# Performance work log

Hardware: AMD Instinct MI355X
Metric: run time of the kernel (lower is better)

The kernel has to match this reference:

```python
import jax, jax.numpy as jnp
import numpy as np

B, S, H = 2, 2048, 2048
NH, HD = 16, 128


def rotate_half(x):
    x1, x2 = x[..., : x.shape[-1] // 2], x[..., x.shape[-1] // 2 :]
    return jnp.concatenate((-x2, x1), axis=-1)


def setup_inputs() -> dict:
    key = jax.random.key(0)
    ks = jax.random.split(key, 8)
    return {
        "hidden": jax.random.normal(ks[0], (B, S, H), dtype=jnp.float32),
        "cos": jax.random.uniform(ks[1], (S, HD), dtype=jnp.float32),
        "sin": jax.random.uniform(ks[2], (S, HD), dtype=jnp.float32),
        "attention_mask": jnp.zeros((B, 1, S, S), dtype=jnp.float32),
        "Wq": jax.random.normal(ks[3], (H, H), dtype=jnp.float32) * 0.02,
        "Wk": jax.random.normal(ks[4], (H, H), dtype=jnp.float32) * 0.02,
        "Wv": jax.random.normal(ks[5], (H, H), dtype=jnp.float32) * 0.02,
        "Wo": jax.random.normal(ks[6], (H, H), dtype=jnp.float32) * 0.02,
    }


def reference(hidden, cos, sin, attention_mask, Wq, Wk, Wv, Wo):
    b, s, h = hidden.shape
    # torch Linear: y = x @ W.T ; reshape to [B, NH, S, HD]
    def proj(W):
        return (hidden @ W.T).reshape(b, s, NH, HD).transpose(0, 2, 1, 3)

    q, k, v = proj(Wq), proj(Wk), proj(Wv)
    c = cos[None, None, :, :]  # [1,1,S,HD]
    si = sin[None, None, :, :]
    q = q * c + rotate_half(q) * si
    k = k * c + rotate_half(k) * si
    scores = jnp.einsum("bhqd,bhkd->bhqk", q, k) / jnp.sqrt(jnp.float32(HD))
    scores = scores + attention_mask
    attn = jax.nn.softmax(scores.astype(jnp.float32), axis=-1).astype(q.dtype)
    out = jnp.einsum("bhqk,bhkd->bhqd", attn, v)
    out = out.transpose(0, 2, 1, 3).reshape(b, s, h)
    return out @ Wo.T
```

## Files before the change

kernel.cpp:

```cpp
#include <hip/hip_runtime.h>
#include <hip/hip_bf16.h>
#include <math.h>

#define SEQ 2048
#define HID 2048
#define NHEAD 16
#define HDIM 128
#define LDQ 6144

typedef __bf16 bf16_t;
typedef __bf16 bf16x2 __attribute__((ext_vector_type(2)));
typedef __bf16 bf16x4_t __attribute__((ext_vector_type(4)));
typedef __bf16 bf16x8 __attribute__((ext_vector_type(8)));
typedef float f32x4 __attribute__((ext_vector_type(4)));
typedef float f32x16 __attribute__((ext_vector_type(16)));
typedef unsigned u32x4 __attribute__((ext_vector_type(4)));

#define MFMA16(a, b, c) __builtin_amdgcn_mfma_f32_16x16x32_bf16(a, b, c, 0, 0, 0)
#define MFMA32(a, b, c) __builtin_amdgcn_mfma_f32_32x32x16_bf16(a, b, c, 0, 0, 0)
#define GLOAD_LDS(g, l) \
  __builtin_amdgcn_global_load_lds((const __attribute__((address_space(1))) void*)(g), \
                                   (__attribute__((address_space(3))) void*)(l), 16, 0, 0)

static __device__ inline unsigned pk2(float lo, float hi) {
  bf16x2 t; t[0] = (bf16_t)lo; t[1] = (bf16_t)hi;
  return __builtin_bit_cast(unsigned, t);
}

__global__ void cast_hidden(const float* __restrict__ in, bf16_t* __restrict__ out) {
  int i = blockIdx.x * 256 + threadIdx.x;
  float4 v = ((const float4*)in)[i];
  bf16x4_t b;
  b[0] = (bf16_t)v.x; b[1] = (bf16_t)v.y; b[2] = (bf16_t)v.z; b[3] = (bf16_t)v.w;
  ((bf16x4_t*)out)[i] = b;
}

__global__ void cast_weights(const float* __restrict__ a, const float* __restrict__ b,
                             const float* __restrict__ c, const float* __restrict__ d,
                             bf16_t* __restrict__ out) {
  const float* srcs[4] = {a, b, c, d};
  const float* src = srcs[blockIdx.y];
  bf16_t* dst = out + (size_t)blockIdx.y * (HID * HID);
  int i = blockIdx.x * 256 + threadIdx.x;
  float4 v = ((const float4*)src)[i];
  bf16x4_t o;
  o[0] = (bf16_t)v.x; o[1] = (bf16_t)v.y; o[2] = (bf16_t)v.z; o[3] = (bf16_t)v.w;
  ((bf16x4_t*)dst)[i] = o;
}

__global__ __launch_bounds__(256, 3) void gemm_bt(
    const bf16_t* __restrict__ A, const bf16_t* __restrict__ Bw,
    bf16_t* __restrict__ Cb, float* __restrict__ Cf,
    int M, int N, int K) {
  __shared__ bf16_t As[2][128 * 32];
  __shared__ bf16_t Bs[2][128 * 32];
  const int tid = threadIdx.x;
  const int lane = tid & 63, wid = tid >> 6;
  const int wr = wid >> 1, wc = wid & 1;
  const int lr = lane & 15, lg = lane >> 4;
  const int nwg = gridDim.x;
  const int lid = (blockIdx.x & 7) * (nwg >> 3) + (blockIdx.x >> 3);
  const int nbc = N >> 7;
  const int brow = lid / nbc, bcol = lid % nbc;

  f32x4 acc[4][4] = {};

  const int srow = tid >> 2, sch = tid & 3;
#define GSTAGE(k0, bb)                                                                   \
  {                                                                                      \
    _Pragma("unroll") for (int is = 0; is < 2; ++is) {                                   \
      int row = srow + is * 64;                                                          \
      GLOAD_LDS(A + (size_t)(brow * 128 + row) * K + (k0) + sch * 8,                     \
                &As[bb][(row * 4 + sch) * 8]);                                           \
      GLOAD_LDS(Bw + (size_t)(bcol * 128 + row) * K + (k0) + sch * 8,                    \
                &Bs[bb][(row * 4 + sch) * 8]);                                           \
    }                                                                                    \
  }

  GSTAGE(0, 0);
  __syncthreads();

  const int nt = K / 32;
  for (int t = 0; t < nt; ++t) {
    const int cb = t & 1;
    if (t + 1 < nt) GSTAGE((t + 1) * 32, cb ^ 1);
    bf16x8 af[4], bfr[4];
#pragma unroll
    for (int m = 0; m < 4; ++m)
      af[m] = *(const bf16x8*)(&As[cb][(wr * 64 + m * 16 + lr) * 32 + lg * 8]);
#pragma unroll
    for (int n = 0; n < 4; ++n)
      bfr[n] = *(const bf16x8*)(&Bs[cb][(wc * 64 + n * 16 + lr) * 32 + lg * 8]);
#pragma unroll
    for (int m = 0; m < 4; ++m)
#pragma unroll
      for (int n = 0; n < 4; ++n)
        acc[m][n] = MFMA16(af[m], bfr[n], acc[m][n]);
    __syncthreads();
  }
#undef GSTAGE

#pragma unroll
  for (int m = 0; m < 4; ++m)
#pragma unroll
    for (int n = 0; n < 4; ++n)
#pragma unroll
      for (int r = 0; r < 4; ++r) {
        int row = brow * 128 + wr * 64 + m * 16 + lg * 4 + r;
        int col = bcol * 128 + wc * 64 + n * 16 + lr;
        float v = acc[m][n][r];
        if (Cf) Cf[(size_t)row * N + col] = v;
        else    Cb[(size_t)row * N + col] = (bf16_t)v;
      }
}

__global__ void rope_qk(bf16_t* __restrict__ QKV,
                        const float* __restrict__ cost, const float* __restrict__ sint) {
  const float SCALE = 0.08838834764831845f;
  int idx = blockIdx.x * 256 + threadIdx.x;
  int d8 = idx & 7;
  int t = idx >> 3;
  int h = t & 15;
  int row = t >> 4;
  int s = row & (SEQ - 1);
  size_t base = (size_t)row * LDQ + h * HDIM;
  const float4* cp = (const float4*)(cost + s * HDIM);
  const float4* sp = (const float4*)(sint + s * HDIM);
  float4 c0a = cp[d8 * 2], c0b = cp[d8 * 2 + 1];
  float4 c1a = cp[16 + d8 * 2], c1b = cp[16 + d8 * 2 + 1];
  float4 s0a = sp[d8 * 2], s0b = sp[d8 * 2 + 1];
  float4 s1a = sp[16 + d8 * 2], s1b = sp[16 + d8 * 2 + 1];
  float c0[8] = {c0a.x, c0a.y, c0a.z, c0a.w, c0b.x, c0b.y, c0b.z, c0b.w};
  float c1[8] = {c1a.x, c1a.y, c1a.z, c1a.w, c1b.x, c1b.y, c1b.z, c1b.w};
  float s0[8] = {s0a.x, s0a.y, s0a.z, s0a.w, s0b.x, s0b.y, s0b.z, s0b.w};
  float s1[8] = {s1a.x, s1a.y, s1a.z, s1a.w, s1b.x, s1b.y, s1b.z, s1b.w};

  bf16_t* Q = QKV;
  bf16_t* K = QKV + 2048;
  bf16x8 qlo = *(bf16x8*)(Q + base + d8 * 8);
  bf16x8 qhi = *(bf16x8*)(Q + base + 64 + d8 * 8);
  bf16x8 klo = *(bf16x8*)(K + base + d8 * 8);
  bf16x8 khi = *(bf16x8*)(K + base + 64 + d8 * 8);
  bf16x8 qlo2, qhi2, klo2, khi2;
#pragma unroll
  for (int j = 0; j < 8; ++j) {
    float q0 = (float)qlo[j], q1 = (float)qhi[j];
    qlo2[j] = (bf16_t)((q0 * c0[j] - q1 * s0[j]) * SCALE);
    qhi2[j] = (bf16_t)((q1 * c1[j] + q0 * s1[j]) * SCALE);
    float k0 = (float)klo[j], k1 = (float)khi[j];
    klo2[j] = (bf16_t)(k0 * c0[j] - k1 * s0[j]);
    khi2[j] = (bf16_t)(k1 * c1[j] + k0 * s1[j]);
  }
  *(bf16x8*)(Q + base + d8 * 8) = qlo2;
  *(bf16x8*)(Q + base + 64 + d8 * 8) = qhi2;
  *(bf16x8*)(K + base + d8 * 8) = klo2;
  *(bf16x8*)(K + base + 64 + d8 * 8) = khi2;
}

__global__ void transpose_v(const bf16_t* __restrict__ Vf, bf16_t* __restrict__ Vt) {
  __shared__ bf16_t t[32][33];
  int tx = threadIdx.x & 31, ty = threadIdx.x >> 5;
  int r0 = blockIdx.y * 32, c0 = blockIdx.x * 32;
#pragma unroll
  for (int j = 0; j < 4; ++j)
    t[ty + j * 8][tx] = Vf[(size_t)(r0 + ty + j * 8) * LDQ + c0 + tx];
  __syncthreads();
#pragma unroll
  for (int j = 0; j < 4; ++j) {
    int c = c0 + ty + j * 8;
    int r = r0 + tx;
    int h = c >> 7, d = c & 127, b = r >> 11, s = r & (SEQ - 1);
    Vt[(((size_t)(b * NHEAD + h)) * HDIM + d) * SEQ + s] = t[tx][ty + j * 8];
  }
}

__global__ __launch_bounds__(512, 2) void flash_fwd(
    const bf16_t* __restrict__ Qf, const bf16_t* __restrict__ Kf,
    const bf16_t* __restrict__ Vt, const float* __restrict__ mask,
    bf16_t* __restrict__ AO) {
  __shared__ char smem[131072];
  char* KsB = smem;
  char* VsB = smem + 65536;
  const int tid = threadIdx.x, lane = tid & 63, wid = tid >> 6;
  const int q32 = lane & 31, hi = lane >> 5;

  const int x = blockIdx.x;
  const int bh = x & 31, qt = x >> 5;
  const int b = bh >> 4, h = bh & 15;
  const int qg = qt * 256 + wid * 32 + q32;

  bf16x8 qf[8];
  const bf16_t* qptr = Qf + (size_t)(b * SEQ + qg) * LDQ + h * HDIM + hi * 8;
#pragma unroll
  for (int ds = 0; ds < 8; ++ds) qf[ds] = *(const bf16x8*)(qptr + ds * 16);

  const float* mp = mask + (size_t)b * SEQ * SEQ + (size_t)qg * SEQ + hi * 4;

  float mrun = -INFINITY, lpart = 0.f;
  f32x16 o[4] = {};

#define STAGE_KV(kt_, bb)                                                                \
  {                                                                                      \
    const int kb0_ = (kt_) * 128;                                                        \
    _Pragma("unroll") for (int is = 0; is < 4; ++is) {                                   \
      int p = tid + is * 512;                                                            \
      int row = p >> 4, ch = p & 15;                                                     \
      int src = (ch * 16) ^ ((row & 7) << 4);                                            \
      GLOAD_LDS((const char*)(Kf + (size_t)(b * SEQ + kb0_ + row) * LDQ + h * HDIM) +    \
                    src,                                                                 \
                KsB + (bb) * 32768 + p * 16);                                            \
      GLOAD_LDS((const char*)(Vt + (size_t)(bh * HDIM + row) * SEQ + kb0_) + src,        \
                VsB + (bb) * 32768 + p * 16);                                            \
    }                                                                                    \
  }

  STAGE_KV(0, 0);
  __syncthreads();

  const int NT = SEQ / 128;
  for (int kt = 0; kt < NT; ++kt) {
    const int cur = kt & 1;
    const int kb0 = kt * 128;
    if (kt + 1 < NT) STAGE_KV(kt + 1, cur ^ 1);

#pragma unroll
    for (int kb = 0; kb < 4; ++kb) {
      f32x16 sacc;
#pragma unroll
      for (int g = 0; g < 4; ++g) {
        float4 m4 = *(const float4*)(mp + kb0 + kb * 32 + 8 * g);
        sacc[4 * g + 0] = m4.x; sacc[4 * g + 1] = m4.y;
        sacc[4 * g + 2] = m4.z; sacc[4 * g + 3] = m4.w;
      }
#pragma unroll
      for (int ds = 0; ds < 8; ++ds) {
        int row = kb * 32 + q32;
        bf16x8 kfr = *(const bf16x8*)(KsB + cur * 32768 + row * 256 +
                                      ((ds * 32 + hi * 16) ^ ((row & 7) << 4)));
        sacc = MFMA32(kfr, qf[ds], sacc);
      }

      float mx = sacc[0];
#pragma unroll
      for (int r = 1; r < 16; ++r) mx = fmaxf(mx, sacc[r]);
      mx = fmaxf(mx, __shfl_xor(mx, 32, 64));
      if (!__all(mx <= mrun + 8.f)) {
        float mnew = fmaxf(mrun, mx);
        float corr = __expf(mrun - mnew);
        mrun = mnew;
        lpart *= corr;
#pragma unroll
        for (int d0 = 0; d0 < 4; ++d0)
#pragma unroll
          for (int r = 0; r < 16; ++r) o[d0][r] *= corr;
      }

      float p[16];
      float rs = 0.f;
#pragma unroll
      for (int r = 0; r < 16; ++r) {
        p[r] = __expf(sacc[r] - mrun);
        rs += p[r];
      }
      lpart += rs;

#pragma unroll
      for (int s = 0; s < 2; ++s) {
        unsigned A1 = pk2(p[8 * s + 0], p[8 * s + 1]);
        unsigned A2 = pk2(p[8 * s + 2], p[8 * s + 3]);
        unsigned B1 = pk2(p[8 * s + 4], p[8 * s + 5]);
        unsigned B2 = pk2(p[8 * s + 6], p[8 * s + 7]);
        unsigned A1s = __shfl_xor(A1, 32, 64);
        unsigned A2s = __shfl_xor(A2, 32, 64);
        unsigned B1s = __shfl_xor(B1, 32, 64);
        unsigned B2s = __shfl_xor(B2, 32, 64);
        unsigned w0 = hi ? B1s : A1;
        unsigned w1 = hi ? B2s : A2;
        unsigned w2 = hi ? B1 : A1s;
        unsigned w3 = hi ? B2 : A2s;
        u32x4 W = {w0, w1, w2, w3};
        bf16x8 pav = __builtin_bit_cast(bf16x8, W);
        const int gs = kb * 2 + s;
#pragma unroll
        for (int d0 = 0; d0 < 4; ++d0) {
          int vrow = d0 * 32 + q32;
          bf16x8 vf = *(const bf16x8*)(VsB + cur * 32768 + vrow * 256 +
                                       ((gs * 32 + hi * 16) ^ ((vrow & 7) << 4)));
          o[d0] = MFMA32(vf, pav, o[d0]);
        }
      }
    }
    __syncthreads();
  }
#undef STAGE_KV

  float l = lpart + __shfl_xor(lpart, 32, 64);
  float rl = 1.f / l;
  bf16_t* aorow = AO + (size_t)(b * SEQ + qg) * HID + h * HDIM;
#pragma unroll
  for (int d0 = 0; d0 < 4; ++d0)
#pragma unroll
    for (int g = 0; g < 4; ++g) {
      unsigned lo = pk2(o[d0][4 * g + 0] * rl, o[d0][4 * g + 1] * rl);
      unsigned hi2 = pk2(o[d0][4 * g + 2] * rl, o[d0][4 * g + 3] * rl);
      int d = d0 * 32 + 8 * g + 4 * hi;
      *(unsigned*)(aorow + d) = lo;
      *(unsigned*)(aorow + d + 2) = hi2;
    }
}

extern "C" void kernel_launch(void* const* d_in, const int* in_sizes, int n_in,
                              void* d_out, int out_size, void* d_ws, size_t ws_size,
                              hipStream_t stream) {
  const float* hidden = (const float*)d_in[0];
  const float* cost   = (const float*)d_in[1];
  const float* sint   = (const float*)d_in[2];
  const float* mask   = (const float*)d_in[3];
  const float* Wq     = (const float*)d_in[4];
  const float* Wk     = (const float*)d_in[5];
  const float* Wv     = (const float*)d_in[6];
  const float* Wo     = (const float*)d_in[7];
  float* out = (float*)d_out;
  char* ws = (char*)d_ws;

  bf16_t* Af  = (bf16_t*)(ws + 0);
  bf16_t* Wqb = (bf16_t*)(ws + 16777216);
  bf16_t* Wob = (bf16_t*)(ws + 41943040);
  bf16_t* QKV = (bf16_t*)(ws + 50331648);
  bf16_t* Vt  = (bf16_t*)(ws + 0);
  bf16_t* AO  = (bf16_t*)(ws + 16777216);

  cast_hidden<<<8192, 256, 0, stream>>>(hidden, Af);
  cast_weights<<<dim3(4096, 4), 256, 0, stream>>>(Wq, Wk, Wv, Wo, Wqb);

  gemm_bt<<<1536, 256, 0, stream>>>(Af, Wqb, QKV, nullptr, 4096, LDQ, HID);

  rope_qk<<<2048, 256, 0, stream>>>(QKV, cost, sint);
  transpose_v<<<dim3(64, 128), 256, 0, stream>>>(QKV + 4096, Vt);

  flash_fwd<<<256, 512, 0, stream>>>(QKV, QKV + 2048, Vt, mask, AO);

  gemm_bt<<<512, 256, 0, stream>>>(AO, Wob, nullptr, out, 4096, HID, HID);
}
```

Before: 331.4 us.

## Use 256x256-tile 8-wave pipelined GEMM for fused QKV projection

Adds a new GEMM kernel with 256x256 output tiles, 512 threads, 128KB LDS double buffering with XOR swizzle, and a phased schedule that interleaves half-tile global-to-LDS loads with MFMA work using setprio and explicit waitcnt/barriers. The QKV projection is switched to it, cutting the grid from 1536 to 384 blocks. Larger tiles raise arithmetic intensity and reduce global/LDS traffic per FLOP. The trade-off is lower occupancy, only 384 blocks on 256 CUs which may leave load imbalance, and fragile hand-tuned wait counts.

Result: faster. 324.8 us (-2.0%).

```diff
diff --git a/kernel.cpp b/kernel.cpp
--- a/kernel.cpp
+++ b/kernel.cpp
@@ -46,6 +46,101 @@
   bf16x4_t o;
   o[0] = (bf16_t)v.x; o[1] = (bf16_t)v.y; o[2] = (bf16_t)v.z; o[3] = (bf16_t)v.w;
   ((bf16x4_t*)dst)[i] = o;
+}
+
+__global__ __launch_bounds__(512, 2) void gemm256(
+    const bf16_t* __restrict__ A, const bf16_t* __restrict__ Bw,
+    bf16_t* __restrict__ Cb, float* __restrict__ Cf, int M, int N, int K) {
+  __shared__ char smem[131072];
+  const int tid = threadIdx.x, lane = tid & 63, wid = tid >> 6;
+  const int wr = wid >> 2, wc = wid & 3;
+  const int lr = lane & 15, lg = lane >> 4;
+  const int nwg = gridDim.x;
+  const int lid = (blockIdx.x & 7) * (nwg >> 3) + (blockIdx.x >> 3);
+  const int nbc = N >> 8;
+  const int brow = lid / nbc, bcol = lid % nbc;
+  const int NT = K >> 6;
+
+  const bf16_t* Ab = A + (size_t)(brow * 256) * K;
+  const bf16_t* Bb = Bw + (size_t)(bcol * 256) * K;
+
+  f32x4 acc[8][4] = {};
+  bf16x8 af[4], bfr[4];
+  const int swz = (lg ^ (lr & 3)) << 4;
+
+#define STAGE_HALF(t_, op, kh)                                                        \
+  {                                                                                   \
+    int tt = (t_) < NT ? (t_) : NT - 1;                                               \
+    const bf16_t* gsrc = (op) ? Bb : Ab;                                              \
+    char* ldst = smem + (tt & 1) * 65536 + (op) * 32768 + (kh) * 16384;               \
+    _Pragma("unroll") for (int is = 0; is < 2; ++is) {                                \
+      int p = tid + is * 512;                                                         \
+      int row = p >> 2, ch = p & 3;                                                   \
+      GLOAD_LDS(gsrc + (size_t)row * K + tt * 64 + (kh) * 32 + ((ch ^ (row & 3)) * 8),\
+                ldst + p * 16);                                                       \
+    }                                                                                 \
+  }
+
+#define PHASE(cb, kh, mh, LOADB, STAGECALL, VM)                                       \
+  {                                                                                   \
+    _Pragma("unroll") for (int mf = 0; mf < 4; ++mf) {                                \
+      int row = wr * 128 + (mh) * 64 + mf * 16 + lr;                                  \
+      af[mf] = *(const bf16x8*)(smem + (cb) * 65536 + (kh) * 16384 + row * 64 + swz); \
+    }                                                                                 \
+    if (LOADB) {                                                                      \
+      _Pragma("unroll") for (int nf = 0; nf < 4; ++nf) {                              \
+        int row = wc * 64 + nf * 16 + lr;                                             \
+        bfr[nf] = *(const bf16x8*)(smem + (cb) * 65536 + 32768 + (kh) * 16384 +       \
+                                   row * 64 + swz);                                   \
+      }                                                                               \
+    }                                                                                 \
+    STAGECALL;                                                                        \
+    __builtin_amdgcn_s_barrier();                                                     \
+    asm volatile("s_waitcnt lgkmcnt(0)" ::: "memory");                                \
+    __builtin_amdgcn_sched_barrier(0);                                                \
+    __builtin_amdgcn_s_setprio(1);                                                    \
+    _Pragma("unroll") for (int mf = 0; mf < 4; ++mf)                                  \
+      _Pragma("unroll") for (int nf = 0; nf < 4; ++nf)                                \
+        acc[(mh) * 4 + mf][nf] = MFMA16(af[mf], bfr[nf], acc[(mh) * 4 + mf][nf]);     \
+    __builtin_amdgcn_s_setprio(0);                                                    \
+    if (VM) { asm volatile("s_waitcnt vmcnt(6)" ::: "memory"); }                      \
+    __builtin_amdgcn_s_barrier();                                                     \
+    __builtin_amdgcn_sched_barrier(0);                                                \
+  }
+
+  STAGE_HALF(0, 1, 0); STAGE_HALF(0, 0, 0); STAGE_HALF(0, 1, 1); STAGE_HALF(0, 0, 1);
+  STAGE_HALF(1, 1, 0); STAGE_HALF(1, 0, 0); STAGE_HALF(1, 1, 1);
+  asm volatile("s_waitcnt vmcnt(6)" ::: "memory");
+  __builtin_amdgcn_s_barrier();
+  __builtin_amdgcn_sched_barrier(0);
+
+  const int NI = NT >> 1;
+  for (int i = 0; i < NI; ++i) {
+    const int t2 = 2 * i;
+    PHASE(0, 0, 0, 1, STAGE_HALF(t2 + 1, 0, 1), 0);
+    PHASE(0, 0, 1, 0, STAGE_HALF(t2 + 2, 1, 0), 0);
+    PHASE(0, 1, 0, 1, STAGE_HALF(t2 + 2, 0, 0), 0);
+    PHASE(0, 1, 1, 0, STAGE_HALF(t2 + 2, 1, 1), 1);
+    PHASE(1, 0, 0, 1, STAGE_HALF(t2 + 2, 0, 1), 0);
+    PHASE(1, 0, 1, 0, STAGE_HALF(t2 + 3, 1, 0), 0);
+    PHASE(1, 1, 0, 1, STAGE_HALF(t2 + 3, 0, 0), 0);
+    PHASE(1, 1, 1, 0, STAGE_HALF(t2 + 3, 1, 1), 1);
+  }
+#undef PHASE
+#undef STAGE_HALF
+
+#pragma unroll
+  for (int mi = 0; mi < 8; ++mi)
+#pragma unroll
+    for (int nf = 0; nf < 4; ++nf)
+#pragma unroll
+      for (int r = 0; r < 4; ++r) {
+        int row = brow * 256 + wr * 128 + (mi >> 2) * 64 + (mi & 3) * 16 + lg * 4 + r;
+        int col = bcol * 256 + wc * 64 + nf * 16 + lr;
+        float v = acc[mi][nf][r];
+        if (Cf) Cf[(size_t)row * N + col] = v;
+        else    Cb[(size_t)row * N + col] = (bf16_t)v;
+      }
 }
 
 __global__ __launch_bounds__(256, 3) void gemm_bt(
@@ -333,7 +428,7 @@
   cast_hidden<<<8192, 256, 0, stream>>>(hidden, Af);
   cast_weights<<<dim3(4096, 4), 256, 0, stream>>>(Wq, Wk, Wv, Wo, Wqb);
 
-  gemm_bt<<<1536, 256, 0, stream>>>(Af, Wqb, QKV, nullptr, 4096, LDQ, HID);
+  gemm256<<<384, 512, 0, stream>>>(Af, Wqb, QKV, nullptr, 4096, LDQ, HID);
 
   rope_qk<<<2048, 256, 0, stream>>>(QKV, cost, sint);
   transpose_v<<<dim3(64, 128), 256, 0, stream>>>(QKV + 4096, Vt);
```
